# Optimization experiments

Hardware: AMD Instinct MI355X
Metric: run time of the kernel (lower is better)

Reference implementation:

```python
import jax, jax.numpy as jnp
import numpy as np

CONF_THRES = 0.5   # self.conf_thres
NMS_THRES = 0.5    # self.nms_thres
PRE_NMS = 2048     # candidates kept before pairwise IoU
MAX_DET = 300      # padded detections returned per image
MAX_WH = 4096.0    # class-offset trick so NMS is per-class
IMG_SIZE = 416.0   # self.img_size; boxes_scale (416,416)->(416,416) => scale 1


def xywh2xyxy(b):
    xy, wh = b[..., :2], b[..., 2:4]
    return jnp.concatenate([xy - wh * 0.5, xy + wh * 0.5], axis=-1)


def pairwise_iou(boxes):
    # boxes: [K,4] xyxy -> [K,K] IoU
    area = (boxes[:, 2] - boxes[:, 0]) * (boxes[:, 3] - boxes[:, 1])
    lt = jnp.maximum(boxes[:, None, :2], boxes[None, :, :2])
    rb = jnp.minimum(boxes[:, None, 2:], boxes[None, :, 2:])
    wh = jnp.clip(rb - lt, 0.0)
    inter = wh[..., 0] * wh[..., 1]
    return inter / (area[:, None] + area[None, :] - inter + 1e-16)


def nms_single(pred):
    # pred: [N,85] = xywh(4) + objectness(1) + class scores(80)
    boxes = xywh2xyxy(pred[:, :4])
    obj = pred[:, 4]
    cls_scores = pred[:, 5:] * obj[:, None]        # conf = obj * class prob
    conf = jnp.max(cls_scores, axis=-1)
    cls_id = jnp.argmax(cls_scores, axis=-1)
    valid = obj >= CONF_THRES                      # confidence threshold filter
    score = jnp.where(valid, conf, -1.0)

    order = jnp.argsort(-score)[:PRE_NMS]          # sort desc, keep top PRE_NMS
    boxes_s = boxes[order]
    score_s = score[order]
    cls_s = cls_id[order]
    valid_s = valid[order]

    # per-class NMS via coordinate offset by class id
    off = cls_s.astype(boxes_s.dtype) * MAX_WH
    iou = pairwise_iou(boxes_s + off[:, None])     # [PRE_NMS, PRE_NMS]

    def body(keep, i):
        suppressed = jnp.any(keep & (iou[:, i] > NMS_THRES))
        k = valid_s[i] & ~suppressed
        return keep.at[i].set(k), k

    keep, _ = jax.lax.scan(body, jnp.zeros(PRE_NMS, dtype=bool), jnp.arange(PRE_NMS))

    final_score = jnp.where(keep, score_s, -1.0)
    top = jnp.argsort(-final_score)[:MAX_DET]
    kb, ks, kc, km = boxes_s[top], score_s[top], cls_s[top], keep[top]

    scale = IMG_SIZE / 416.0                       # boxes_scale (identity here)
    det = jnp.concatenate(
        [kb * scale, ks[:, None], kc[:, None].astype(kb.dtype)], axis=-1)
    return jnp.where(km[:, None], det, 0.0)        # [MAX_DET, 6] padded


def setup_inputs() -> dict:
    key = jax.random.key(0)
    predictions = jax.random.uniform(key, (16, 10647, 85), dtype=jnp.float32)
    return {"predictions": predictions}


def reference(predictions):
    # detections per image: [x1,y1,x2,y2,score,class], zero-padded to MAX_DET
    return jax.vmap(nms_single)(predictions)  # [B, MAX_DET, 6]
```

## Files before the change

kernel.cpp:

```cpp
#include <hip/hip_runtime.h>
#include <hip/hip_bf16.h>
#include <stdint.h>

typedef unsigned long long u64;
typedef unsigned int u32;
typedef unsigned short u16;

#define NANCH 10647
#define NBATCH 16
#define NSORT 16384
#define NSEL 2048
#define NWORD 32
#define NCLS 80
#define CONF_T 0.5f
#define NMS_T 0.5f
#define MAXDET 300
#define MAXWH 4096.0f
#define CANDCAP 10688

__global__ __launch_bounds__(1024) void k_zero(u32* __restrict__ p, int nwords) {
    for (int i = threadIdx.x; i < nwords; i += 1024) p[i] = 0;
}

__global__ __launch_bounds__(256) void k_prep(const float* __restrict__ pred,
                                              u64* __restrict__ keys,
                                              float4* __restrict__ boxes,
                                              int* __restrict__ cls,
                                              float* __restrict__ score,
                                              u32* __restrict__ ghist) {
    __shared__ float sm[128 * 85];
    __shared__ u32 ph[256];
    int b = blockIdx.y;
    int a0 = blockIdx.x * 128;
    int na = NANCH - a0; if (na > 128) na = 128;
    const float* src = pred + ((size_t)b * NANCH + a0) * 85;
    int tot = na * 85;
    ph[threadIdx.x] = 0;
    for (int i = threadIdx.x; i < tot; i += 256) sm[i] = src[i];
    __syncthreads();
    int t = threadIdx.x;
    u64 kk = 0;
    if (t < na) {
        const float* s = &sm[t * 85];
        float x = s[0], y = s[1], w = s[2], h = s[3], obj = s[4];
        float best = s[5] * obj; int arg = 0;
        #pragma unroll
        for (int c = 1; c < 80; ++c) {
            float v = s[5 + c] * obj;
            if (v > best) { best = v; arg = c; }
        }
        bool valid = obj >= CONF_T;
        float sc = valid ? best : -1.0f;
        int a = a0 + t;
        float4 bx;
        bx.x = x - w * 0.5f; bx.y = y - h * 0.5f;
        bx.z = x + w * 0.5f; bx.w = y + h * 0.5f;
        size_t o = (size_t)b * NANCH + a;
        boxes[o] = bx;
        cls[o] = arg;
        score[o] = sc;
        u32 u = __float_as_uint(sc);
        u32 v = (u & 0x80000000u) ? ~u : (u | 0x80000000u);
        u32 hi = ~v;
        kk = ((u64)hi << 32) | (u32)a;
        keys[(size_t)b * NSORT + a] = kk;
    }
    u32 bin = (t < na) ? (u32)(kk >> 56) : 0xFFFFFFFFu;
    int lane = t & 63;
    u64 rem = __ballot(t < na);
    while (rem) {
        int srcl = __ffsll((long long)rem) - 1;
        u32 lb = __shfl(bin, srcl);
        u64 same = __ballot(bin == lb) & rem;
        if (lane == srcl) atomicAdd(&ph[lb], (u32)__popcll(same));
        rem &= ~same;
    }
    __syncthreads();
    if (ph[threadIdx.x]) atomicAdd(&ghist[(size_t)b * 256 + threadIdx.x], ph[threadIdx.x]);
}

__global__ __launch_bounds__(1024) void k_sel(const u64* __restrict__ keys,
                                              const u32* __restrict__ ghist,
                                              const float4* __restrict__ boxes,
                                              const int* __restrict__ cls,
                                              const float* __restrict__ score,
                                              float4* __restrict__ sel_box,
                                              float4* __restrict__ sel_sbox,
                                              float* __restrict__ sel_area,
                                              float* __restrict__ sel_score,
                                              int* __restrict__ sel_cls) {
    __shared__ u64 sk[NSEL];
    __shared__ u64 cand[CANDCAP];
    __shared__ u32 hist[256];
    __shared__ u32 hsc[256];
    __shared__ u64 s_red[16];
    __shared__ u32 s_D0, s_D, s_rank, s_cnt, s_cand;

    int b = blockIdx.x;
    int tid = threadIdx.x;
    int lane = tid & 63;
    u64 below = (1ULL << lane) - 1ULL;
    const u64* KB = keys + (size_t)b * NSORT;

    if (tid == 0) { s_cnt = 0; s_cand = 0; }
    for (int i = tid; i < NSEL; i += 1024) sk[i] = ~0ULL;
    if (tid < 256) hist[tid] = ghist[(size_t)b * 256 + tid];
    __syncthreads();
    if (tid < 64) {
        u32 h0 = hist[tid*4], h1 = hist[tid*4+1], h2 = hist[tid*4+2], h3 = hist[tid*4+3];
        u32 loc = h0 + h1 + h2 + h3;
        u32 p = loc;
        #pragma unroll
        for (int o = 1; o < 64; o <<= 1) { u32 t2 = __shfl_up(p, o); if (lane >= o) p += t2; }
        u32 base = p - loc;
        hsc[tid*4]   = base + h0;
        hsc[tid*4+1] = base + h0 + h1;
        hsc[tid*4+2] = base + h0 + h1 + h2;
        hsc[tid*4+3] = base + h0 + h1 + h2 + h3;
    }
    __syncthreads();
    if (tid < 256) {
        u32 inc = hsc[tid], cb = inc - hist[tid];
        if (cb < NSEL && NSEL <= inc) { s_D0 = tid; s_rank = NSEL - cb; }
    }
    __syncthreads();
    u32 D0 = s_D0;

    for (int it = 0; it < 11; ++it) {
        int i = tid + it * 1024;
        bool inb = i < NANCH;
        u64 kk = inb ? KB[i] : 0ULL;
        u32 top = (u32)(kk >> 56);
        bool is_s = inb && (top < D0);
        bool is_c = inb && (top == D0);
        u64 bs = __ballot(is_s), bc = __ballot(is_c);
        u32 base_s = 0, base_c = 0;
        if (lane == 0) {
            if (bs) base_s = atomicAdd(&s_cnt, (u32)__popcll(bs));
            if (bc) base_c = atomicAdd(&s_cand, (u32)__popcll(bc));
        }
        base_s = __shfl(base_s, 0); base_c = __shfl(base_c, 0);
        if (is_s) sk[base_s + __popcll(bs & below)] = kk;
        if (is_c) cand[base_c + __popcll(bc & below)] = kk;
    }
    __syncthreads();

    const int shifts2[5] = {48, 40, 32, 8, 0};
    for (int rr = 0; ; ++rr) {
        u32 cn = s_cand, r = s_rank;
        if (r == cn || rr == 5) {
            for (u32 i0 = 0; i0 < cn; i0 += 1024) {
                u32 i = i0 + tid;
                bool take = i < cn;
                u64 kk = take ? cand[i] : 0ULL;
                u64 bt = __ballot(take);
                u32 base = 0;
                if (lane == 0 && bt) base = atomicAdd(&s_cnt, (u32)__popcll(bt));
                base = __shfl(base, 0);
                if (take) sk[base + __popcll(bt & below)] = kk;
            }
            break;
        }
        if (r == 1) {
            u64 best = ~0ULL;
            for (u32 i = tid; i < cn; i += 1024) { u64 kk = cand[i]; if (kk < best) best = kk; }
            #pragma unroll
            for (int o = 32; o > 0; o >>= 1) {
                u64 other = __shfl_down(best, o);
                if (other < best) best = other;
            }
            if (lane == 0) s_red[tid >> 6] = best;
            __syncthreads();
            if (tid == 0) {
                u64 m = s_red[0];
                for (int w2 = 1; w2 < 16; ++w2) if (s_red[w2] < m) m = s_red[w2];
                sk[atomicAdd(&s_cnt, 1u)] = m;
            }
            break;
        }
        int shift = shifts2[rr];
        if (tid < 256) hist[tid] = 0;
        __syncthreads();
        for (u32 i = tid; i < cn; i += 1024)
            atomicAdd(&hist[(u32)(cand[i] >> shift) & 0xFFu], 1u);
        __syncthreads();
        if (tid < 64) {
            u32 h0 = hist[tid*4], h1 = hist[tid*4+1], h2 = hist[tid*4+2], h3 = hist[tid*4+3];
            u32 loc = h0 + h1 + h2 + h3;
            u32 p = loc;
            #pragma unroll
            for (int o = 1; o < 64; o <<= 1) { u32 t2 = __shfl_up(p, o); if (lane >= o) p += t2; }
            u32 base = p - loc;
            hsc[tid*4]   = base + h0;
            hsc[tid*4+1] = base + h0 + h1;
            hsc[tid*4+2] = base + h0 + h1 + h2;
            hsc[tid*4+3] = base + h0 + h1 + h2 + h3;
        }
        __syncthreads();
        if (tid < 256) {
            u32 inc = hsc[tid], cb = inc - hist[tid];
            if (cb < r && r <= inc) { s_D = tid; s_rank = r - cb; }
        }
        __syncthreads();
        u32 D = s_D;
        u64 mk[11], mc[11]; int nk = 0, nc = 0;
        for (u32 i = tid; i < cn; i += 1024) {
            u64 kk = cand[i];
            u32 dg = (u32)(kk >> shift) & 0xFFu;
            if (dg < D) mk[nk++] = kk;
            else if (dg == D) mc[nc++] = kk;
        }
        __syncthreads();
        if (tid == 0) s_cand = 0;
        __syncthreads();
        if (nk) { u32 p = atomicAdd(&s_cnt, (u32)nk); for (int j = 0; j < nk; ++j) sk[p + j] = mk[j]; }
        if (nc) { u32 p = atomicAdd(&s_cand, (u32)nc); for (int j = 0; j < nc; ++j) cand[p + j] = mc[j]; }
        __syncthreads();
    }
    __syncthreads();

    {
        int w = tid >> 6, l = lane;
        int base = w * 128;
        u64 a = sk[base + l], c = sk[base + 64 + l];
        #pragma unroll
        for (int k = 2; k <= 128; k <<= 1) {
            for (int j = k >> 1; j > 0; j >>= 1) {
                if (j == 64) {
                    bool dir = (((base + l) & k) == 0);
                    u64 lo = a < c ? a : c;
                    u64 hi = a < c ? c : a;
                    a = dir ? lo : hi;
                    c = dir ? hi : lo;
                } else {
                    bool up_ = (l & j) != 0;
                    bool dira = (((base + l) & k) == 0);
                    bool dirc = (((base + 64 + l) & k) == 0);
                    u64 pa = __shfl_xor(a, j);
                    u64 pc = __shfl_xor(c, j);
                    a = (up_ == dira) ? (a > pa ? a : pa) : (a < pa ? a : pa);
                    c = (up_ == dirc) ? (c > pc ? c : pc) : (c < pc ? c : pc);
                }
            }
        }
        sk[base + l] = a; sk[base + 64 + l] = c;
        __syncthreads();
        for (int k = 256; k <= NSEL; k <<= 1) {
            for (int j = k >> 1; j >= 128; j >>= 1) {
                int n = tid;
                int i = ((n & ~(j - 1)) << 1) | (n & (j - 1));
                int l2 = i | j;
                u64 x = sk[i], y = sk[l2];
                bool up2 = ((i & k) == 0);
                if ((x > y) == up2) { sk[i] = y; sk[l2] = x; }
                __syncthreads();
            }
            a = sk[base + l]; c = sk[base + 64 + l];
            bool dirk = ((base & k) == 0);
            {
                u64 lo = a < c ? a : c;
                u64 hi = a < c ? c : a;
                a = dirk ? lo : hi;
                c = dirk ? hi : lo;
            }
            #pragma unroll
            for (int j = 32; j > 0; j >>= 1) {
                bool up_ = (l & j) != 0;
                u64 pa = __shfl_xor(a, j);
                u64 pc = __shfl_xor(c, j);
                a = (up_ == dirk) ? (a > pa ? a : pa) : (a < pa ? a : pa);
                c = (up_ == dirk) ? (c > pc ? c : pc) : (c < pc ? c : pc);
            }
            sk[base + l] = a; sk[base + 64 + l] = c;
            __syncthreads();
        }
    }

    for (int r2 = tid; r2 < NSEL; r2 += 1024) {
        u64 key = sk[r2];
        int a = (int)(key & 0xFFFFFFFFu);
        if ((unsigned)a >= NANCH) a = 0;
        size_t src = (size_t)b * NANCH + a;
        float4 bx = boxes[src];
        int c = cls[src];
        float sc = score[src];
        float off = (float)c * MAXWH;
        float4 sb;
        sb.x = bx.x + off; sb.y = bx.y + off;
        sb.z = bx.z + off; sb.w = bx.w + off;
        float area = (sb.z - sb.x) * (sb.w - sb.y);
        size_t o = (size_t)b * NSEL + r2;
        sel_box[o] = bx; sel_sbox[o] = sb; sel_area[o] = area;
        sel_score[o] = sc; sel_cls[o] = c;
    }
}

__global__ __launch_bounds__(1024) void k_cnms(const float4* __restrict__ sel_sbox,
                                               const float* __restrict__ sel_area,
                                               const int* __restrict__ sel_cls,
                                               const float* __restrict__ sel_score,
                                               u64* __restrict__ gkeep) {
    __shared__ u16 wmem[16][NSEL];
    __shared__ u64 wkeep[16][NWORD];

    int b = blockIdx.y;
    int cg = blockIdx.x;
    int lane = threadIdx.x & 63, wv = threadIdx.x >> 6;
    int c = cg * 16 + wv;
    size_t bb = (size_t)b * NSEL;
    const int* CL = sel_cls + bb;
    const float* SC = sel_score + bb;
    u64 below = (1ULL << lane) - 1ULL;

    int n = 0;
    for (int ch = 0; ch < NWORD; ++ch) {
        int i = ch * 64 + lane;
        bool pred = (CL[i] == c) && (SC[i] >= 0.0f);
        u64 bal = __ballot(pred);
        if (pred) wmem[wv][n + __popcll(bal & below)] = (u16)i;
        n += __popcll(bal);
    }

    for (int c0 = 0; c0 < n; c0 += 64) {
        int chunkn = n - c0; if (chunkn > 64) chunkn = 64;
        bool mv = lane < chunkn;
        int q = mv ? (int)wmem[wv][c0 + lane] : 0;
        float4 bq = sel_sbox[bb + q];
        float aq = sel_area[bb + q];

        bool hit = false;
        for (int j = 0; j < c0; ++j) {
            if (!((wkeep[wv][j >> 6] >> (j & 63)) & 1ULL)) continue;
            int p = (int)wmem[wv][j];
            float4 bp = sel_sbox[bb + p];
            float ap = sel_area[bb + p];
            float ltx = fmaxf(bp.x, bq.x), lty = fmaxf(bp.y, bq.y);
            float rbx = fminf(bp.z, bq.z), rby = fminf(bp.w, bq.w);
            float ww = fmaxf(rbx - ltx, 0.0f), hh = fmaxf(rby - lty, 0.0f);
            float inter = ww * hh;
            hit = hit || (mv && (inter / (ap + aq - inter + 1e-16f) > NMS_T));
        }
        u64 avail = __ballot(mv && !hit);

        u64 Rt = 0;
        for (int t = 0; t < chunkn; ++t) {
            int p = (int)wmem[wv][c0 + t];
            float4 bp = sel_sbox[bb + p];
            float ap = sel_area[bb + p];
            float ltx = fmaxf(bp.x, bq.x), lty = fmaxf(bp.y, bq.y);
            float rbx = fminf(bp.z, bq.z), rby = fminf(bp.w, bq.w);
            float ww = fmaxf(rbx - ltx, 0.0f), hh = fmaxf(rby - lty, 0.0f);
            float inter = ww * hh;
            u64 row = __ballot(mv && (inter / (ap + aq - inter + 1e-16f) > NMS_T));
            if (lane == t) Rt = row;
        }

        u64 U = avail, kept = 0;
        while (U) {
            bool inU = ((U >> lane) & 1ULL) != 0ULL;
            u64 newk = __ballot(inU && ((Rt & U & below) == 0ULL));
            u64 killed = __ballot((Rt & newk) != 0ULL);
            kept |= newk;
            U &= ~(newk | killed);
        }
        if (lane == 0) wkeep[wv][c0 >> 6] = kept;
        if ((kept >> lane) & 1ULL)
            atomicOr(&gkeep[(size_t)b * NWORD + (q >> 6)], 1ULL << (q & 63));
    }
}

__global__ __launch_bounds__(64) void k_out(const u64* __restrict__ gkeep,
                                            const float4* __restrict__ sel_box,
                                            const float* __restrict__ sel_score,
                                            const int* __restrict__ sel_cls,
                                            float* __restrict__ out) {
    int b = blockIdx.x;
    int lane = threadIdx.x;
    const float* SC = sel_score + (size_t)b * NSEL;
    u64 kreg = (lane < NWORD) ? gkeep[(size_t)b * NWORD + lane] : 0ULL;

    int cnt = (lane < NWORD) ? __popcll(kreg) : 0;
    int pre = cnt;
    #pragma unroll
    for (int dd = 1; dd < 64; dd <<= 1) {
        int o = __shfl_up(pre, dd);
        if (lane >= dd) pre += o;
    }
    int total = __shfl(pre, 63);
    int base = pre - cnt;
    float* OUT = out + (size_t)b * MAXDET * 6;
    if (lane < NWORD) {
        u64 m = kreg;
        int rr = 0;
        while (m) {
            int t = __ffsll((long long)m) - 1;
            m &= m - 1;
            int slot = base + rr; ++rr;
            if (slot < MAXDET) {
                int i = lane * 64 + t;
                size_t src = (size_t)b * NSEL + i;
                float4 bx = sel_box[src];
                float sc = SC[i];
                int c = sel_cls[src];
                float* o6 = OUT + slot * 6;
                o6[0] = bx.x; o6[1] = bx.y; o6[2] = bx.z; o6[3] = bx.w;
                o6[4] = sc; o6[5] = (float)c;
            }
        }
    }
    int start = total > MAXDET ? MAXDET : total;
    for (int s = start + lane; s < MAXDET; s += 64) {
        float* o6 = OUT + s * 6;
        o6[0] = 0.0f; o6[1] = 0.0f; o6[2] = 0.0f;
        o6[3] = 0.0f; o6[4] = 0.0f; o6[5] = 0.0f;
    }
}

extern "C" void kernel_launch(void* const* d_in, const int* in_sizes, int n_in,
                              void* d_out, int out_size, void* d_ws, size_t ws_size,
                              hipStream_t stream) {
    const float* pred = (const float*)d_in[0];
    float* out = (float*)d_out;

    char* ws = (char*)d_ws;
    size_t off = 0;
    auto alloc = [&](size_t bytes) -> void* {
        void* p = ws + off;
        off += (bytes + 255) & ~(size_t)255;
        return p;
    };

    u64*    keys      = (u64*)   alloc((size_t)NBATCH * NSORT * 8);
    float4* boxes     = (float4*)alloc((size_t)NBATCH * NANCH * 16);
    int*    cls       = (int*)   alloc((size_t)NBATCH * NANCH * 4);
    float*  score     = (float*) alloc((size_t)NBATCH * NANCH * 4);
    float4* sel_box   = (float4*)alloc((size_t)NBATCH * NSEL * 16);
    float4* sel_sbox  = (float4*)alloc((size_t)NBATCH * NSEL * 16);
    float*  sel_area  = (float*) alloc((size_t)NBATCH * NSEL * 4);
    float*  sel_score = (float*) alloc((size_t)NBATCH * NSEL * 4);
    int*    sel_cls   = (int*)   alloc((size_t)NBATCH * NSEL * 4);
    u64*    gkeep     = (u64*)   alloc((size_t)NBATCH * NWORD * 8);
    u32*    ghist     = (u32*)   alloc((size_t)NBATCH * 256 * 4);

    int zwords = (int)(((size_t)NBATCH * NWORD * 8 + (size_t)NBATCH * 256 * 4) / 4);
    k_zero<<<1, 1024, 0, stream>>>((u32*)gkeep, zwords);

    dim3 g1((NANCH + 127) / 128, NBATCH);
    k_prep<<<g1, 256, 0, stream>>>(pred, keys, boxes, cls, score, ghist);

    k_sel<<<NBATCH, 1024, 0, stream>>>(keys, ghist, boxes, cls, score,
                                       sel_box, sel_sbox, sel_area,
                                       sel_score, sel_cls);

    dim3 g3(5, NBATCH);
    k_cnms<<<g3, 1024, 0, stream>>>(sel_sbox, sel_area, sel_cls, sel_score, gkeep);

    k_out<<<NBATCH, 64, 0, stream>>>(gkeep, sel_box, sel_score, sel_cls, out);
}
```

Baseline: 109.4 us.

## Split top-k selection into multi-block scan, finalize, and parallel gather kernels

The single per-image selection kernel is split in three. A scan kernel spreads the first radix pass over 8 blocks per image using global atomic counters. A finalize kernel runs the remaining radix refinement and bitonic sort per image. A separate gather kernel fetches the selected boxes across more blocks. The refinement loop also switches to ballot-based compaction instead of per-thread register lists. This raises parallelism in the key scan and gather, at the cost of two extra launches and round trips through global memory.

```diff
diff --git a/kernel.cpp b/kernel.cpp
--- a/kernel.cpp
+++ b/kernel.cpp
@@ -17,6 +17,7 @@
 #define MAXDET 300
 #define MAXWH 4096.0f
 #define CANDCAP 10688
+#define PART 1344
 
 __global__ __launch_bounds__(1024) void k_zero(u32* __restrict__ p, int nwords) {
     for (int i = threadIdx.x; i < nwords; i += 1024) p[i] = 0;
@@ -79,31 +80,22 @@
     if (ph[threadIdx.x]) atomicAdd(&ghist[(size_t)b * 256 + threadIdx.x], ph[threadIdx.x]);
 }
 
-__global__ __launch_bounds__(1024) void k_sel(const u64* __restrict__ keys,
-                                              const u32* __restrict__ ghist,
-                                              const float4* __restrict__ boxes,
-                                              const int* __restrict__ cls,
-                                              const float* __restrict__ score,
-                                              float4* __restrict__ sel_box,
-                                              float4* __restrict__ sel_sbox,
-                                              float* __restrict__ sel_area,
-                                              float* __restrict__ sel_score,
-                                              int* __restrict__ sel_cls) {
-    __shared__ u64 sk[NSEL];
-    __shared__ u64 cand[CANDCAP];
+__global__ __launch_bounds__(1024) void k_scan(const u64* __restrict__ keys,
+                                               const u32* __restrict__ ghist,
+                                               u64* __restrict__ gsk,
+                                               u64* __restrict__ gcand,
+                                               u32* __restrict__ gcnt,
+                                               u32* __restrict__ gcandcnt) {
     __shared__ u32 hist[256];
     __shared__ u32 hsc[256];
-    __shared__ u64 s_red[16];
-    __shared__ u32 s_D0, s_D, s_rank, s_cnt, s_cand;
-
-    int b = blockIdx.x;
+    __shared__ u32 s_D0;
+    int b = blockIdx.y;
+    int part = blockIdx.x;
     int tid = threadIdx.x;
     int lane = tid & 63;
     u64 below = (1ULL << lane) - 1ULL;
     const u64* KB = keys + (size_t)b * NSORT;
 
-    if (tid == 0) { s_cnt = 0; s_cand = 0; }
-    for (int i = tid; i < NSEL; i += 1024) sk[i] = ~0ULL;
     if (tid < 256) hist[tid] = ghist[(size_t)b * 256 + tid];
     __syncthreads();
     if (tid < 64) {
@@ -121,14 +113,18 @@
     __syncthreads();
     if (tid < 256) {
         u32 inc = hsc[tid], cb = inc - hist[tid];
-        if (cb < NSEL && NSEL <= inc) { s_D0 = tid; s_rank = NSEL - cb; }
+        if (cb < NSEL && NSEL <= inc) s_D0 = tid;
     }
     __syncthreads();
     u32 D0 = s_D0;
 
-    for (int it = 0; it < 11; ++it) {
-        int i = tid + it * 1024;
-        bool inb = i < NANCH;
+    u64* SKB = gsk + (size_t)b * NSEL;
+    u64* CDB = gcand + (size_t)b * CANDCAP;
+    #pragma unroll
+    for (int it = 0; it < 2; ++it) {
+        int off = it * 1024 + tid;
+        int i = part * PART + off;
+        bool inb = (off < PART) && (i < NANCH);
         u64 kk = inb ? KB[i] : 0ULL;
         u32 top = (u32)(kk >> 56);
         bool is_s = inb && (top < D0);
@@ -136,13 +132,39 @@
         u64 bs = __ballot(is_s), bc = __ballot(is_c);
         u32 base_s = 0, base_c = 0;
         if (lane == 0) {
-            if (bs) base_s = atomicAdd(&s_cnt, (u32)__popcll(bs));
-            if (bc) base_c = atomicAdd(&s_cand, (u32)__popcll(bc));
+            if (bs) base_s = atomicAdd(&gcnt[b], (u32)__popcll(bs));
+            if (bc) base_c = atomicAdd(&gcandcnt[b], (u32)__popcll(bc));
         }
         base_s = __shfl(base_s, 0); base_c = __shfl(base_c, 0);
-        if (is_s) sk[base_s + __popcll(bs & below)] = kk;
-        if (is_c) cand[base_c + __popcll(bc & below)] = kk;
-    }
+        if (is_s) SKB[base_s + __popcll(bs & below)] = kk;
+        if (is_c) CDB[base_c + __popcll(bc & below)] = kk;
+    }
+}
+
+__global__ __launch_bounds__(1024) void k_fin(const u64* __restrict__ gsk,
+                                              const u64* __restrict__ gcand,
+                                              const u32* __restrict__ gcnt,
+                                              const u32* __restrict__ gcandcnt,
+                                              u64* __restrict__ gskey) {
+    __shared__ u64 sk[NSEL];
+    __shared__ u64 cand[CANDCAP];
+    __shared__ u32 hist[256];
+    __shared__ u32 hsc[256];
+    __shared__ u64 s_red[16];
+    __shared__ u32 s_D, s_rank, s_cnt, s_cand;
+
+    int b = blockIdx.x;
+    int tid = threadIdx.x;
+    int lane = tid & 63;
+    u64 below = (1ULL << lane) - 1ULL;
+
+    u32 skn = gcnt[b];
+    u32 cn0 = gcandcnt[b];
+    if (tid == 0) { s_cnt = skn; s_rank = NSEL - skn; s_cand = cn0; }
+    for (int i = tid; i < NSEL; i += 1024)
+        sk[i] = (i < (int)skn) ? gsk[(size_t)b * NSEL + i] : ~0ULL;
+    for (u32 i = tid; i < cn0; i += 1024)
+        cand[i] = gcand[(size_t)b * CANDCAP + i];
     __syncthreads();
 
     const int shifts2[5] = {48, 40, 32, 8, 0};
@@ -203,18 +225,36 @@
         }
         __syncthreads();
         u32 D = s_D;
-        u64 mk[11], mc[11]; int nk = 0, nc = 0;
-        for (u32 i = tid; i < cn; i += 1024) {
-            u64 kk = cand[i];
-            u32 dg = (u32)(kk >> shift) & 0xFFu;
-            if (dg < D) mk[nk++] = kk;
-            else if (dg == D) mc[nc++] = kk;
+        u64 vv[11]; bool vb[11];
+        #pragma unroll
+        for (int it = 0; it < 11; ++it) {
+            u32 i = tid + it * 1024;
+            vb[it] = (i < cn);
+            vv[it] = vb[it] ? cand[i] : 0ULL;
         }
         __syncthreads();
         if (tid == 0) s_cand = 0;
         __syncthreads();
-        if (nk) { u32 p = atomicAdd(&s_cnt, (u32)nk); for (int j = 0; j < nk; ++j) sk[p + j] = mk[j]; }
-        if (nc) { u32 p = atomicAdd(&s_cand, (u32)nc); for (int j = 0; j < nc; ++j) cand[p + j] = mc[j]; }
+        #pragma unroll
+        for (int it = 0; it < 11; ++it) {
+            u32 dg = (u32)(vv[it] >> shift) & 0xFFu;
+            bool tk = vb[it] && (dg < D);
+            u64 bt = __ballot(tk);
+            u32 base = 0;
+            if (lane == 0 && bt) base = atomicAdd(&s_cnt, (u32)__popcll(bt));
+            base = __shfl(base, 0);
+            if (tk) sk[base + __popcll(bt & below)] = vv[it];
+        }
+        #pragma unroll
+        for (int it = 0; it < 11; ++it) {
+            u32 dg = (u32)(vv[it] >> shift) & 0xFFu;
+            bool tk = vb[it] && (dg == D);
+            u64 bt = __ballot(tk);
+            u32 base = 0;
+            if (lane == 0 && bt) base = atomicAdd(&s_cand, (u32)__popcll(bt));
+            base = __shfl(base, 0);
+            if (tk) cand[base + __popcll(bt & below)] = vv[it];
+        }
         __syncthreads();
     }
     __syncthreads();
@@ -276,23 +316,35 @@
         }
     }
 
-    for (int r2 = tid; r2 < NSEL; r2 += 1024) {
-        u64 key = sk[r2];
-        int a = (int)(key & 0xFFFFFFFFu);
-        if ((unsigned)a >= NANCH) a = 0;
-        size_t src = (size_t)b * NANCH + a;
-        float4 bx = boxes[src];
-        int c = cls[src];
-        float sc = score[src];
-        float off = (float)c * MAXWH;
-        float4 sb;
-        sb.x = bx.x + off; sb.y = bx.y + off;
-        sb.z = bx.z + off; sb.w = bx.w + off;
-        float area = (sb.z - sb.x) * (sb.w - sb.y);
-        size_t o = (size_t)b * NSEL + r2;
-        sel_box[o] = bx; sel_sbox[o] = sb; sel_area[o] = area;
-        sel_score[o] = sc; sel_cls[o] = c;
-    }
+    for (int i = tid; i < NSEL; i += 1024) gskey[(size_t)b * NSEL + i] = sk[i];
+}
+
+__global__ __launch_bounds__(256) void k_gather(const u64* __restrict__ gskey,
+                                                const float4* __restrict__ boxes,
+                                                const int* __restrict__ cls,
+                                                const float* __restrict__ score,
+                                                float4* __restrict__ sel_box,
+                                                float4* __restrict__ sel_sbox,
+                                                float* __restrict__ sel_area,
+                                                float* __restrict__ sel_score,
+                                                int* __restrict__ sel_cls) {
+    int b = blockIdx.y;
+    int r = blockIdx.x * 256 + threadIdx.x;
+    u64 key = gskey[(size_t)b * NSEL + r];
+    int a = (int)(key & 0xFFFFFFFFu);
+    if ((unsigned)a >= NANCH) a = 0;
+    size_t src = (size_t)b * NANCH + a;
+    float4 bx = boxes[src];
+    int c = cls[src];
+    float sc = score[src];
+    float off = (float)c * MAXWH;
+    float4 sb;
+    sb.x = bx.x + off; sb.y = bx.y + off;
+    sb.z = bx.z + off; sb.w = bx.w + off;
+    float area = (sb.z - sb.x) * (sb.w - sb.y);
+    size_t o = (size_t)b * NSEL + r;
+    sel_box[o] = bx; sel_sbox[o] = sb; sel_area[o] = area;
+    sel_score[o] = sc; sel_cls[o] = c;
 }
 
 __global__ __launch_bounds__(1024) void k_cnms(const float4* __restrict__ sel_sbox,
@@ -439,21 +491,32 @@
     float*  sel_area  = (float*) alloc((size_t)NBATCH * NSEL * 4);
     float*  sel_score = (float*) alloc((size_t)NBATCH * NSEL * 4);
     int*    sel_cls   = (int*)   alloc((size_t)NBATCH * NSEL * 4);
+    u64*    gsk       = (u64*)   alloc((size_t)NBATCH * NSEL * 8);
+    u64*    gcand     = (u64*)   alloc((size_t)NBATCH * CANDCAP * 8);
+    u64*    gskey     = (u64*)   alloc((size_t)NBATCH * NSEL * 8);
     u64*    gkeep     = (u64*)   alloc((size_t)NBATCH * NWORD * 8);
     u32*    ghist     = (u32*)   alloc((size_t)NBATCH * 256 * 4);
-
-    int zwords = (int)(((size_t)NBATCH * NWORD * 8 + (size_t)NBATCH * 256 * 4) / 4);
-    k_zero<<<1, 1024, 0, stream>>>((u32*)gkeep, zwords);
+    u32*    gcnt      = (u32*)   alloc((size_t)NBATCH * 4);
+    u32*    gcandcnt  = (u32*)   alloc((size_t)NBATCH * 4);
+
+    size_t zbytes = (char*)(gcandcnt + NBATCH) - (char*)gkeep;
+    k_zero<<<1, 1024, 0, stream>>>((u32*)gkeep, (int)(zbytes / 4));
 
     dim3 g1((NANCH + 127) / 128, NBATCH);
     k_prep<<<g1, 256, 0, stream>>>(pred, keys, boxes, cls, score, ghist);
 
-    k_sel<<<NBATCH, 1024, 0, stream>>>(keys, ghist, boxes, cls, score,
-                                       sel_box, sel_sbox, sel_area,
-                                       sel_score, sel_cls);
-
-    dim3 g3(5, NBATCH);
-    k_cnms<<<g3, 1024, 0, stream>>>(sel_sbox, sel_area, sel_cls, sel_score, gkeep);
+    dim3 g2(8, NBATCH);
+    k_scan<<<g2, 1024, 0, stream>>>(keys, ghist, gsk, gcand, gcnt, gcandcnt);
+
+    k_fin<<<NBATCH, 1024, 0, stream>>>(gsk, gcand, gcnt, gcandcnt, gskey);
+
+    dim3 g4(8, NBATCH);
+    k_gather<<<g4, 256, 0, stream>>>(gskey, boxes, cls, score,
+                                     sel_box, sel_sbox, sel_area,
+                                     sel_score, sel_cls);
+
+    dim3 g5(5, NBATCH);
+    k_cnms<<<g5, 1024, 0, stream>>>(sel_sbox, sel_area, sel_cls, sel_score, gkeep);
 
     k_out<<<NBATCH, 64, 0, stream>>>(gkeep, sel_box, sel_score, sel_cls, out);
 }
```

New measurement: 134.3 us. 1.23x slower.
